# Performance work log

Hardware: AMD Instinct MI355X
Metric: run time of the kernel (lower is better)

The kernel has to match this reference:

```python
import jax, jax.numpy as jnp
import numpy as np

N, IN_DIM, HID, OUT = 8192, 512, 256, 64
NEG_INF = -9e15


def setup_inputs() -> dict:
    key = jax.random.key(0)
    ks = jax.random.split(key, 7)
    X = jax.random.normal(ks[0], (N, IN_DIM), dtype=jnp.float32)
    A = jax.random.randint(ks[1], (N, N), 0, 2, dtype=jnp.int32)
    # fc1 (Linear): kaiming-uniform-ish init, exact dist irrelevant for correctness
    W1 = jax.random.normal(ks[2], (IN_DIM, HID), dtype=jnp.float32) / np.sqrt(IN_DIM)
    b1 = jnp.zeros((HID,), dtype=jnp.float32)
    # attention vector a: xavier_uniform(gain=1.414) on shape (2*HID, 1)
    lim = 1.414 * np.sqrt(6.0 / (2 * HID + 1))
    a = jax.random.uniform(ks[3], (2 * HID, 1), minval=-lim, maxval=lim, dtype=jnp.float32)
    Omega = jax.random.normal(ks[4], (HID, OUT), dtype=jnp.float32) * np.sqrt(2.0 / (HID + OUT))
    beta = jnp.zeros((OUT,), dtype=jnp.float32)
    return {"X": X, "A": A, "W1": W1, "b1": b1, "a": a, "Omega": Omega, "beta": beta}


def reference(X, A, W1, b1, a, Omega, beta):
    H1 = X @ W1 + b1                      # [N, HID]
    # score(i,j) = leakyrelu(a[:HID].H1_i + a[HID:].H1_j) -- computed via broadcast,
    # avoiding the O(N^2 * 2*HID) concat the torch code materializes.
    a1 = a[:HID, 0]                       # [HID]
    a2 = a[HID:, 0]                       # [HID]
    e = jax.nn.leaky_relu((H1 @ a1)[:, None] + (H1 @ a2)[None, :], negative_slope=0.2)  # [N, N]
    e = jnp.where(A > 0, e, NEG_INF)
    attention = jax.nn.softmax(e, axis=1)  # dropout_rate=0.0 -> identity
    H2 = attention @ H1                    # [N, HID]
    return jax.nn.sigmoid(H2 @ Omega + beta)  # [N, OUT]
```

## Files before the change

kernel.cpp:

```cpp
#include <hip/hip_runtime.h>
#include <hip/hip_bf16.h>


typedef float f32x4 __attribute__((ext_vector_type(4)));
typedef short s16x8 __attribute__((ext_vector_type(8)));

#define NN 8192
#define INDIM 512
#define HIDD 256
#define OUTD 64

static __device__ __forceinline__ short f2bf(float x) {
    __hip_bfloat16 h = __float2bfloat16(x);
    return __builtin_bit_cast(short, h);
}

static __device__ __forceinline__ void split_bf(float x, short& hi, short& lo) {
    short h = f2bf(x);
    unsigned int hb = ((unsigned int)(unsigned short)h) << 16;
    float hf = __builtin_bit_cast(float, hb);
    hi = h;
    lo = f2bf(x - hf);
}

__global__ void k_splitW1(const float* __restrict__ W1,
                          short* __restrict__ W1Thi, short* __restrict__ W1Tlo) {
    int t = blockIdx.x * 256 + threadIdx.x;
    int n = t >> 9;
    int k = t & 511;
    float x = W1[k * 256 + n];
    short hi, lo; split_bf(x, hi, lo);
    W1Thi[t] = hi;
    W1Tlo[t] = lo;
}

__global__ void __launch_bounds__(256, 2)
k_h1(const float* __restrict__ X, const short* __restrict__ W1Thi,
     const short* __restrict__ W1Tlo, const float* __restrict__ b1,
     const float* __restrict__ avec, unsigned short* __restrict__ H1TB,
     float* __restrict__ alw, float* __restrict__ bew, float* __restrict__ uvw) {
    __shared__ float s1p[4][16];
    __shared__ float s2p[4][16];
    const int tid = threadIdx.x;
    const int wn = tid >> 6, lane = tid & 63;
    const int q = lane >> 4, m16 = lane & 15;
    const int i0 = blockIdx.x * 16;
    const int irow = i0 + m16;

    f32x4 zero4 = {0.f, 0.f, 0.f, 0.f};
    f32x4 acc[4];
#pragma unroll
    for (int nt = 0; nt < 4; ++nt) acc[nt] = zero4;

    const float* Xrow = X + (size_t)irow * INDIM;
    for (int kk = 0; kk < INDIM; kk += 32) {
        const int k0 = kk + q * 8;
        float4 xa = *(const float4*)(Xrow + k0);
        float4 xb = *(const float4*)(Xrow + k0 + 4);
        float xs[8] = {xa.x, xa.y, xa.z, xa.w, xb.x, xb.y, xb.z, xb.w};
        s16x8 ahi, alo;
#pragma unroll
        for (int j = 0; j < 8; ++j) { short h, l; split_bf(xs[j], h, l); ahi[j] = h; alo[j] = l; }
#pragma unroll
        for (int nt = 0; nt < 4; ++nt) {
            const int n = wn * 64 + nt * 16 + m16;
            s16x8 bhi = *(const s16x8*)(W1Thi + n * INDIM + k0);
            s16x8 blo = *(const s16x8*)(W1Tlo + n * INDIM + k0);
            acc[nt] = __builtin_amdgcn_mfma_f32_16x16x32_bf16(ahi, bhi, acc[nt], 0, 0, 0);
            acc[nt] = __builtin_amdgcn_mfma_f32_16x16x32_bf16(ahi, blo, acc[nt], 0, 0, 0);
            acc[nt] = __builtin_amdgcn_mfma_f32_16x16x32_bf16(alo, bhi, acc[nt], 0, 0, 0);
        }
    }

    float p1[4] = {0.f, 0.f, 0.f, 0.f};
    float p2[4] = {0.f, 0.f, 0.f, 0.f};
    const int rowbase = i0 + q * 4;
    const int chunk = rowbase >> 5, win = rowbase & 31;
#pragma unroll
    for (int nt = 0; nt < 4; ++nt) {
        const int col = wn * 64 + nt * 16 + m16;
        const float b1v = b1[col];
        const float a1v = avec[col];
        const float a2v = avec[HIDD + col];
        float v0 = acc[nt][0] + b1v;
        float v1 = acc[nt][1] + b1v;
        float v2 = acc[nt][2] + b1v;
        float v3 = acc[nt][3] + b1v;
        ushort4 us;
        us.x = (unsigned short)f2bf(v0);
        us.y = (unsigned short)f2bf(v1);
        us.z = (unsigned short)f2bf(v2);
        us.w = (unsigned short)f2bf(v3);
        *(ushort4*)(H1TB + (size_t)chunk * 8192 + col * 32 + win) = us;
        p1[0] += v0 * a1v; p1[1] += v1 * a1v; p1[2] += v2 * a1v; p1[3] += v3 * a1v;
        p2[0] += v0 * a2v; p2[1] += v1 * a2v; p2[2] += v2 * a2v; p2[3] += v3 * a2v;
    }
#pragma unroll
    for (int off = 1; off < 16; off <<= 1) {
#pragma unroll
        for (int r = 0; r < 4; ++r) {
            p1[r] += __shfl_xor(p1[r], off);
            p2[r] += __shfl_xor(p2[r], off);
        }
    }
    if (m16 == 0) {
#pragma unroll
        for (int r = 0; r < 4; ++r) {
            s1p[wn][q * 4 + r] = p1[r];
            s2p[wn][q * 4 + r] = p2[r];
        }
    }
    __syncthreads();
    if (tid < 16) {
        const int i = i0 + tid;
        float s1 = s1p[0][tid] + s1p[1][tid] + s1p[2][tid] + s1p[3][tid];
        float s2 = s2p[0][tid] + s2p[1][tid] + s2p[2][tid] + s2p[3][tid];
        alw[i] = expf(s1);
        bew[i] = expf(0.2f * s1);
        uvw[2 * i]     = expf(s2);
        uvw[2 * i + 1] = expf(0.2f * s2);
    }
}

__global__ void __launch_bounds__(256, 4)
k_attn(const int* __restrict__ A, const unsigned short* __restrict__ H1TB,
       const float* __restrict__ alw, const float* __restrict__ bew,
       const float* __restrict__ uvw,
       float* __restrict__ H2acc, float* __restrict__ Zw) {
    __shared__ unsigned short tile[8192];

    const int tid = threadIdx.x;
    const int wave = tid >> 6, lane = tid & 63;
    const int q = lane >> 4, m16 = lane & 15;
    const int wm = wave & 1, wn = wave >> 1;
    const int mb = blockIdx.x & 255;
    const int ks = blockIdx.x >> 8;
    const int i = mb * 32 + wm * 16 + m16;
    const float al = alw[i], be = bew[i];

    const unsigned short* gp = H1TB + (size_t)ks * 64 * 8192 + tid * 8;
    __attribute__((address_space(3))) unsigned short* tl =
        (__attribute__((address_space(3))) unsigned short*)tile;

    const int* Ap = A + (size_t)i * NN + ks * 2048 + q * 8;
    const float* uvp = uvw + 2 * (ks * 2048 + q * 8);

    f32x4 zero4 = {0.f, 0.f, 0.f, 0.f};
    f32x4 acc[8];
#pragma unroll
    for (int nt = 0; nt < 8; ++nt) acc[nt] = zero4;
    float zacc = 0.f;

    for (int kk = 0; kk < 2048; kk += 32) {
#pragma unroll
        for (int c = 0; c < 4; ++c)
            __builtin_amdgcn_global_load_lds(
                (const __attribute__((address_space(1))) void*)(gp + c * 2048),
                (__attribute__((address_space(3))) void*)(tl + c * 2048 + tid * 8),
                16, 0, 0);
        gp += 8192;

        int4 A0 = *(const int4*)(Ap);
        int4 A1 = *(const int4*)(Ap + 4);
        float4 uv0 = *(const float4*)(uvp);
        float4 uv1 = *(const float4*)(uvp + 4);
        float4 uv2 = *(const float4*)(uvp + 8);
        float4 uv3 = *(const float4*)(uvp + 12);
        Ap += 32; uvp += 64;

        float wv[8];
        wv[0] = (A0.x > 0) ? fmaxf(al * uv0.x, be * uv0.y) : 0.f;
        wv[1] = (A0.y > 0) ? fmaxf(al * uv0.z, be * uv0.w) : 0.f;
        wv[2] = (A0.z > 0) ? fmaxf(al * uv1.x, be * uv1.y) : 0.f;
        wv[3] = (A0.w > 0) ? fmaxf(al * uv1.z, be * uv1.w) : 0.f;
        wv[4] = (A1.x > 0) ? fmaxf(al * uv2.x, be * uv2.y) : 0.f;
        wv[5] = (A1.y > 0) ? fmaxf(al * uv2.z, be * uv2.w) : 0.f;
        wv[6] = (A1.z > 0) ? fmaxf(al * uv3.x, be * uv3.y) : 0.f;
        wv[7] = (A1.w > 0) ? fmaxf(al * uv3.z, be * uv3.w) : 0.f;
        zacc += (wv[0] + wv[1] + wv[2] + wv[3]) + (wv[4] + wv[5] + wv[6] + wv[7]);
        s16x8 af;
#pragma unroll
        for (int j = 0; j < 8; ++j) af[j] = f2bf(wv[j]);

        __syncthreads();
#pragma unroll
        for (int nt = 0; nt < 8; ++nt) {
            s16x8 bf = *(const s16x8*)(tile + (wn * 128 + nt * 16 + m16) * 32 + q * 8);
            acc[nt] = __builtin_amdgcn_mfma_f32_16x16x32_bf16(af, bf, acc[nt], 0, 0, 0);
        }
        __syncthreads();
    }

    zacc += __shfl_xor(zacc, 16);
    zacc += __shfl_xor(zacc, 32);
    if (wn == 0 && q == 0) atomicAdd(&Zw[i], zacc);

    const int rowbase = mb * 32 + wm * 16 + q * 4;
#pragma unroll
    for (int nt = 0; nt < 8; ++nt) {
        const int col = wn * 128 + nt * 16 + m16;
#pragma unroll
        for (int r = 0; r < 4; ++r)
            atomicAdd(&H2acc[(size_t)(rowbase + r) * HIDD + col], acc[nt][r]);
    }
}

__global__ void __launch_bounds__(256)
k_out(const float* __restrict__ H2acc, const float* __restrict__ Zw,
      const float* __restrict__ Omega, const float* __restrict__ beta,
      float* __restrict__ out) {
    __shared__ float om[HIDD * OUTD];
    const int tid = threadIdx.x;
    for (int idx = tid; idx < HIDD * OUTD; idx += 256) om[idx] = Omega[idx];
    __syncthreads();
    const int wave = tid >> 6, o = tid & 63;
    const float bv = beta[o];
    for (int rr = 0; rr < 8; ++rr) {
        const int i = blockIdx.x * 32 + wave * 8 + rr;
        const float4* H2v = (const float4*)(H2acc + (size_t)i * HIDD);
        float acc = 0.f;
#pragma unroll 4
        for (int c4 = 0; c4 < 64; ++c4) {
            float4 h = H2v[c4];
            const int cb = c4 * 4;
            acc = fmaf(h.x, om[(cb + 0) * OUTD + o], acc);
            acc = fmaf(h.y, om[(cb + 1) * OUTD + o], acc);
            acc = fmaf(h.z, om[(cb + 2) * OUTD + o], acc);
            acc = fmaf(h.w, om[(cb + 3) * OUTD + o], acc);
        }
        const float zinv = 1.0f / Zw[i];
        const float logit = acc * zinv + bv;
        out[(size_t)i * OUTD + o] = 1.0f / (1.0f + expf(-logit));
    }
}

extern "C" void kernel_launch(void* const* d_in, const int* in_sizes, int n_in,
                              void* d_out, int out_size, void* d_ws, size_t ws_size,
                              hipStream_t stream) {
    const float* X     = (const float*)d_in[0];
    const int*   A     = (const int*)d_in[1];
    const float* W1    = (const float*)d_in[2];
    const float* b1    = (const float*)d_in[3];
    const float* avec  = (const float*)d_in[4];
    const float* Omega = (const float*)d_in[5];
    const float* beta  = (const float*)d_in[6];
    float* out = (float*)d_out;

    char* ws = (char*)d_ws;
    unsigned short* H1TB = (unsigned short*)(ws + 0);
    short* W1Thi = (short*)(ws + 4194304);
    short* W1Tlo = (short*)(ws + 4456448);
    float* alw   = (float*)(ws + 4718592);
    float* bew   = (float*)(ws + 4751360);
    float* uvw   = (float*)(ws + 4784128);
    float* Zw    = (float*)(ws + 4849664);
    float* H2acc = (float*)(ws + 4882432);

    hipMemsetAsync(Zw, 0, 32768 + 8388608, stream);

    k_splitW1<<<512, 256, 0, stream>>>(W1, W1Thi, W1Tlo);
    k_h1<<<512, 256, 0, stream>>>(X, W1Thi, W1Tlo, b1, avec, H1TB, alw, bew, uvw);
    k_attn<<<1024, 256, 0, stream>>>(A, H1TB, alw, bew, uvw, H2acc, Zw);
    k_out<<<256, 256, 0, stream>>>(H2acc, Zw, Omega, beta, out);
}
```

Baseline: 543.9 us.

## Pre-tile X and W1 into MFMA fragment layout, drop LDS in attention kernel

Adds prep kernels that convert X to bf16 (high part only) and W1 to hi/lo bf16, both stored in MFMA-fragment-contiguous layout, so the H1 GEMM does two MFMAs per step instead of three. The X low part is dropped, which lowers the precision of H1. The attention kernel no longer stages H1 through LDS with barriers. Each wave now handles two row groups and reads B fragments straight from global memory in a blocked layout, with A loads prefetched one step ahead and the K range split into 8 slices. The output kernel is restructured to reuse Omega loads across 8 rows, and the workspace is aliased so XBhi shares space with Zw/H2acc, with the memset moved after k_h1.

Measured after the change: 566.3 us. 1.04x slower.

```diff
diff --git a/kernel.cpp b/kernel.cpp
--- a/kernel.cpp
+++ b/kernel.cpp
@@ -23,20 +23,25 @@
     lo = f2bf(x - hf);
 }
 
-__global__ void k_splitW1(const float* __restrict__ W1,
-                          short* __restrict__ W1Thi, short* __restrict__ W1Tlo) {
+__global__ void k_prepX(const float* __restrict__ X, short* __restrict__ XBhi) {
     int t = blockIdx.x * 256 + threadIdx.x;
-    int n = t >> 9;
-    int k = t & 511;
-    float x = W1[k * 256 + n];
-    short hi, lo; split_bf(x, hi, lo);
-    W1Thi[t] = hi;
-    W1Tlo[t] = lo;
+    int r = t >> 9, k = t & 511;
+    XBhi[(r >> 4) * 8192 + (k >> 3) * 128 + (r & 15) * 8 + (k & 7)] = f2bf(X[t]);
+}
+
+__global__ void k_prepW(const float* __restrict__ W1,
+                        short* __restrict__ WBhi, short* __restrict__ WBlo) {
+    int t = blockIdx.x * 256 + threadIdx.x;
+    int k = t >> 8, n = t & 255;
+    short h, l; split_bf(W1[t], h, l);
+    int idx = (n >> 4) * 8192 + (k >> 3) * 128 + (n & 15) * 8 + (k & 7);
+    WBhi[idx] = h;
+    WBlo[idx] = l;
 }
 
 __global__ void __launch_bounds__(256, 2)
-k_h1(const float* __restrict__ X, const short* __restrict__ W1Thi,
-     const short* __restrict__ W1Tlo, const float* __restrict__ b1,
+k_h1(const short* __restrict__ XBhi, const short* __restrict__ WBhi,
+     const short* __restrict__ WBlo, const float* __restrict__ b1,
      const float* __restrict__ avec, unsigned short* __restrict__ H1TB,
      float* __restrict__ alw, float* __restrict__ bew, float* __restrict__ uvw) {
     __shared__ float s1p[4][16];
@@ -44,38 +49,30 @@
     const int tid = threadIdx.x;
     const int wn = tid >> 6, lane = tid & 63;
     const int q = lane >> 4, m16 = lane & 15;
-    const int i0 = blockIdx.x * 16;
-    const int irow = i0 + m16;
+    const int blk = blockIdx.x;
 
     f32x4 zero4 = {0.f, 0.f, 0.f, 0.f};
     f32x4 acc[4];
 #pragma unroll
     for (int nt = 0; nt < 4; ++nt) acc[nt] = zero4;
 
-    const float* Xrow = X + (size_t)irow * INDIM;
-    for (int kk = 0; kk < INDIM; kk += 32) {
-        const int k0 = kk + q * 8;
-        float4 xa = *(const float4*)(Xrow + k0);
-        float4 xb = *(const float4*)(Xrow + k0 + 4);
-        float xs[8] = {xa.x, xa.y, xa.z, xa.w, xb.x, xb.y, xb.z, xb.w};
-        s16x8 ahi, alo;
-#pragma unroll
-        for (int j = 0; j < 8; ++j) { short h, l; split_bf(xs[j], h, l); ahi[j] = h; alo[j] = l; }
+    const short* xh = XBhi + blk * 8192 + q * 128 + m16 * 8;
+    const short* wh = WBhi + wn * 4 * 8192 + q * 128 + m16 * 8;
+    const short* wl = WBlo + wn * 4 * 8192 + q * 128 + m16 * 8;
+
+    for (int c = 0; c < 16; ++c) {
+        s16x8 ahi = *(const s16x8*)(xh + c * 512);
 #pragma unroll
         for (int nt = 0; nt < 4; ++nt) {
-            const int n = wn * 64 + nt * 16 + m16;
-            s16x8 bhi = *(const s16x8*)(W1Thi + n * INDIM + k0);
-            s16x8 blo = *(const s16x8*)(W1Tlo + n * INDIM + k0);
+            s16x8 bhi = *(const s16x8*)(wh + nt * 8192 + c * 512);
+            s16x8 blo = *(const s16x8*)(wl + nt * 8192 + c * 512);
             acc[nt] = __builtin_amdgcn_mfma_f32_16x16x32_bf16(ahi, bhi, acc[nt], 0, 0, 0);
             acc[nt] = __builtin_amdgcn_mfma_f32_16x16x32_bf16(ahi, blo, acc[nt], 0, 0, 0);
-            acc[nt] = __builtin_amdgcn_mfma_f32_16x16x32_bf16(alo, bhi, acc[nt], 0, 0, 0);
         }
     }
 
     float p1[4] = {0.f, 0.f, 0.f, 0.f};
     float p2[4] = {0.f, 0.f, 0.f, 0.f};
-    const int rowbase = i0 + q * 4;
-    const int chunk = rowbase >> 5, win = rowbase & 31;
 #pragma unroll
     for (int nt = 0; nt < 4; ++nt) {
         const int col = wn * 64 + nt * 16 + m16;
@@ -91,7 +88,9 @@
         us.y = (unsigned short)f2bf(v1);
         us.z = (unsigned short)f2bf(v2);
         us.w = (unsigned short)f2bf(v3);
-        *(ushort4*)(H1TB + (size_t)chunk * 8192 + col * 32 + win) = us;
+        const int idx = ((wn * 4 + nt) * 1024 + blk * 2 + (q >> 1)) * 128
+                        + m16 * 8 + (q & 1) * 4;
+        *(ushort4*)(H1TB + idx) = us;
         p1[0] += v0 * a1v; p1[1] += v1 * a1v; p1[2] += v2 * a1v; p1[3] += v3 * a1v;
         p2[0] += v0 * a2v; p2[1] += v1 * a2v; p2[2] += v2 * a2v; p2[3] += v3 * a2v;
     }
@@ -112,7 +111,7 @@
     }
     __syncthreads();
     if (tid < 16) {
-        const int i = i0 + tid;
+        const int i = blk * 16 + tid;
         float s1 = s1p[0][tid] + s1p[1][tid] + s1p[2][tid] + s1p[3][tid];
         float s2 = s2p[0][tid] + s2p[1][tid] + s2p[2][tid] + s2p[3][tid];
         alw[i] = expf(s1);
@@ -127,81 +126,96 @@
        const float* __restrict__ alw, const float* __restrict__ bew,
        const float* __restrict__ uvw,
        float* __restrict__ H2acc, float* __restrict__ Zw) {
-    __shared__ unsigned short tile[8192];
-
     const int tid = threadIdx.x;
-    const int wave = tid >> 6, lane = tid & 63;
+    const int wn = tid >> 6, lane = tid & 63;
     const int q = lane >> 4, m16 = lane & 15;
-    const int wm = wave & 1, wn = wave >> 1;
-    const int mb = blockIdx.x & 255;
-    const int ks = blockIdx.x >> 8;
-    const int i = mb * 32 + wm * 16 + m16;
-    const float al = alw[i], be = bew[i];
-
-    const unsigned short* gp = H1TB + (size_t)ks * 64 * 8192 + tid * 8;
-    __attribute__((address_space(3))) unsigned short* tl =
-        (__attribute__((address_space(3))) unsigned short*)tile;
-
-    const int* Ap = A + (size_t)i * NN + ks * 2048 + q * 8;
-    const float* uvp = uvw + 2 * (ks * 2048 + q * 8);
+    const int ks = blockIdx.x & 7;
+    const int mb = blockIdx.x >> 3;
+    const int row0 = mb * 32 + m16, row1 = row0 + 16;
+    const float al0 = alw[row0], be0 = bew[row0];
+    const float al1 = alw[row1], be1 = bew[row1];
+    const int j0 = ks * 1024;
+
+    const int* Ap0 = A + (size_t)row0 * NN + j0 + q * 8;
+    const int* Ap1 = A + (size_t)row1 * NN + j0 + q * 8;
+    const float* uvp = uvw + 2 * (j0 + q * 8);
+    const unsigned short* Hp = H1TB + ((size_t)(wn * 4) * 1024 + ks * 128 + q) * 128 + m16 * 8;
 
     f32x4 zero4 = {0.f, 0.f, 0.f, 0.f};
     f32x4 acc[8];
 #pragma unroll
-    for (int nt = 0; nt < 8; ++nt) acc[nt] = zero4;
-    float zacc = 0.f;
-
-    for (int kk = 0; kk < 2048; kk += 32) {
-#pragma unroll
-        for (int c = 0; c < 4; ++c)
-            __builtin_amdgcn_global_load_lds(
-                (const __attribute__((address_space(1))) void*)(gp + c * 2048),
-                (__attribute__((address_space(3))) void*)(tl + c * 2048 + tid * 8),
-                16, 0, 0);
-        gp += 8192;
-
-        int4 A0 = *(const int4*)(Ap);
-        int4 A1 = *(const int4*)(Ap + 4);
+    for (int i = 0; i < 8; ++i) acc[i] = zero4;
+    float z0 = 0.f, z1 = 0.f;
+
+    int4 a00 = *(const int4*)(Ap0);
+    int4 a01 = *(const int4*)(Ap0 + 4);
+    int4 a10 = *(const int4*)(Ap1);
+    int4 a11 = *(const int4*)(Ap1 + 4);
+
+    for (int t = 0; t < 32; ++t) {
+        int4 n00, n01, n10, n11;
+        if (t < 31) {
+            n00 = *(const int4*)(Ap0 + 32);
+            n01 = *(const int4*)(Ap0 + 36);
+            n10 = *(const int4*)(Ap1 + 32);
+            n11 = *(const int4*)(Ap1 + 36);
+        }
         float4 uv0 = *(const float4*)(uvp);
         float4 uv1 = *(const float4*)(uvp + 4);
         float4 uv2 = *(const float4*)(uvp + 8);
         float4 uv3 = *(const float4*)(uvp + 12);
-        Ap += 32; uvp += 64;
-
-        float wv[8];
-        wv[0] = (A0.x > 0) ? fmaxf(al * uv0.x, be * uv0.y) : 0.f;
-        wv[1] = (A0.y > 0) ? fmaxf(al * uv0.z, be * uv0.w) : 0.f;
-        wv[2] = (A0.z > 0) ? fmaxf(al * uv1.x, be * uv1.y) : 0.f;
-        wv[3] = (A0.w > 0) ? fmaxf(al * uv1.z, be * uv1.w) : 0.f;
-        wv[4] = (A1.x > 0) ? fmaxf(al * uv2.x, be * uv2.y) : 0.f;
-        wv[5] = (A1.y > 0) ? fmaxf(al * uv2.z, be * uv2.w) : 0.f;
-        wv[6] = (A1.z > 0) ? fmaxf(al * uv3.x, be * uv3.y) : 0.f;
-        wv[7] = (A1.w > 0) ? fmaxf(al * uv3.z, be * uv3.w) : 0.f;
-        zacc += (wv[0] + wv[1] + wv[2] + wv[3]) + (wv[4] + wv[5] + wv[6] + wv[7]);
-        s16x8 af;
-#pragma unroll
-        for (int j = 0; j < 8; ++j) af[j] = f2bf(wv[j]);
-
-        __syncthreads();
-#pragma unroll
-        for (int nt = 0; nt < 8; ++nt) {
-            s16x8 bf = *(const s16x8*)(tile + (wn * 128 + nt * 16 + m16) * 32 + q * 8);
-            acc[nt] = __builtin_amdgcn_mfma_f32_16x16x32_bf16(af, bf, acc[nt], 0, 0, 0);
-        }
-        __syncthreads();
-    }
-
-    zacc += __shfl_xor(zacc, 16);
-    zacc += __shfl_xor(zacc, 32);
-    if (wn == 0 && q == 0) atomicAdd(&Zw[i], zacc);
-
-    const int rowbase = mb * 32 + wm * 16 + q * 4;
-#pragma unroll
-    for (int nt = 0; nt < 8; ++nt) {
-        const int col = wn * 128 + nt * 16 + m16;
-#pragma unroll
-        for (int r = 0; r < 4; ++r)
-            atomicAdd(&H2acc[(size_t)(rowbase + r) * HIDD + col], acc[nt][r]);
+
+        float w0[8], w1[8];
+        w0[0] = (a00.x > 0) ? fmaxf(al0 * uv0.x, be0 * uv0.y) : 0.f;
+        w0[1] = (a00.y > 0) ? fmaxf(al0 * uv0.z, be0 * uv0.w) : 0.f;
+        w0[2] = (a00.z > 0) ? fmaxf(al0 * uv1.x, be0 * uv1.y) : 0.f;
+        w0[3] = (a00.w > 0) ? fmaxf(al0 * uv1.z, be0 * uv1.w) : 0.f;
+        w0[4] = (a01.x > 0) ? fmaxf(al0 * uv2.x, be0 * uv2.y) : 0.f;
+        w0[5] = (a01.y > 0) ? fmaxf(al0 * uv2.z, be0 * uv2.w) : 0.f;
+        w0[6] = (a01.z > 0) ? fmaxf(al0 * uv3.x, be0 * uv3.y) : 0.f;
+        w0[7] = (a01.w > 0) ? fmaxf(al0 * uv3.z, be0 * uv3.w) : 0.f;
+        w1[0] = (a10.x > 0) ? fmaxf(al1 * uv0.x, be1 * uv0.y) : 0.f;
+        w1[1] = (a10.y > 0) ? fmaxf(al1 * uv0.z, be1 * uv0.w) : 0.f;
+        w1[2] = (a10.z > 0) ? fmaxf(al1 * uv1.x, be1 * uv1.y) : 0.f;
+        w1[3] = (a10.w > 0) ? fmaxf(al1 * uv1.z, be1 * uv1.w) : 0.f;
+        w1[4] = (a11.x > 0) ? fmaxf(al1 * uv2.x, be1 * uv2.y) : 0.f;
+        w1[5] = (a11.y > 0) ? fmaxf(al1 * uv2.z, be1 * uv2.w) : 0.f;
+        w1[6] = (a11.z > 0) ? fmaxf(al1 * uv3.x, be1 * uv3.y) : 0.f;
+        w1[7] = (a11.w > 0) ? fmaxf(al1 * uv3.z, be1 * uv3.w) : 0.f;
+        z0 += (w0[0] + w0[1] + w0[2] + w0[3]) + (w0[4] + w0[5] + w0[6] + w0[7]);
+        z1 += (w1[0] + w1[1] + w1[2] + w1[3]) + (w1[4] + w1[5] + w1[6] + w1[7]);
+
+        s16x8 af0, af1;
+#pragma unroll
+        for (int j = 0; j < 8; ++j) { af0[j] = f2bf(w0[j]); af1[j] = f2bf(w1[j]); }
+
+#pragma unroll
+        for (int nt = 0; nt < 4; ++nt) {
+            s16x8 bf = *(const s16x8*)(Hp + (size_t)nt * 131072 + t * 512);
+            acc[nt * 2 + 0] = __builtin_amdgcn_mfma_f32_16x16x32_bf16(af0, bf, acc[nt * 2 + 0], 0, 0, 0);
+            acc[nt * 2 + 1] = __builtin_amdgcn_mfma_f32_16x16x32_bf16(af1, bf, acc[nt * 2 + 1], 0, 0, 0);
+        }
+        if (t < 31) { a00 = n00; a01 = n01; a10 = n10; a11 = n11; }
+        Ap0 += 32; Ap1 += 32; uvp += 64;
+    }
+
+    z0 += __shfl_xor(z0, 16); z0 += __shfl_xor(z0, 32);
+    z1 += __shfl_xor(z1, 16); z1 += __shfl_xor(z1, 32);
+    if (wn == 0 && q == 0) {
+        atomicAdd(&Zw[row0], z0);
+        atomicAdd(&Zw[row1], z1);
+    }
+
+#pragma unroll
+    for (int nt = 0; nt < 4; ++nt) {
+        const int col = wn * 64 + nt * 16 + m16;
+#pragma unroll
+        for (int rg = 0; rg < 2; ++rg) {
+            const int rowb = mb * 32 + rg * 16 + q * 4;
+#pragma unroll
+            for (int r = 0; r < 4; ++r)
+                atomicAdd(&H2acc[(size_t)(rowb + r) * HIDD + col], acc[nt * 2 + rg][r]);
+        }
     }
 }
 
@@ -214,23 +228,24 @@
     for (int idx = tid; idx < HIDD * OUTD; idx += 256) om[idx] = Omega[idx];
     __syncthreads();
     const int wave = tid >> 6, o = tid & 63;
+    const int i0 = blockIdx.x * 32 + wave * 8;
+    float acc[8] = {0.f, 0.f, 0.f, 0.f, 0.f, 0.f, 0.f, 0.f};
+    for (int c = 0; c < HIDD; c += 4) {
+        const float o0 = om[(c + 0) * OUTD + o];
+        const float o1 = om[(c + 1) * OUTD + o];
+        const float o2 = om[(c + 2) * OUTD + o];
+        const float o3 = om[(c + 3) * OUTD + o];
+#pragma unroll
+        for (int r = 0; r < 8; ++r) {
+            float4 h = *(const float4*)(H2acc + (size_t)(i0 + r) * HIDD + c);
+            acc[r] = fmaf(h.x, o0, fmaf(h.y, o1, fmaf(h.z, o2, fmaf(h.w, o3, acc[r]))));
+        }
+    }
     const float bv = beta[o];
-    for (int rr = 0; rr < 8; ++rr) {
-        const int i = blockIdx.x * 32 + wave * 8 + rr;
-        const float4* H2v = (const float4*)(H2acc + (size_t)i * HIDD);
-        float acc = 0.f;
-#pragma unroll 4
-        for (int c4 = 0; c4 < 64; ++c4) {
-            float4 h = H2v[c4];
-            const int cb = c4 * 4;
-            acc = fmaf(h.x, om[(cb + 0) * OUTD + o], acc);
-            acc = fmaf(h.y, om[(cb + 1) * OUTD + o], acc);
-            acc = fmaf(h.z, om[(cb + 2) * OUTD + o], acc);
-            acc = fmaf(h.w, om[(cb + 3) * OUTD + o], acc);
-        }
-        const float zinv = 1.0f / Zw[i];
-        const float logit = acc * zinv + bv;
-        out[(size_t)i * OUTD + o] = 1.0f / (1.0f + expf(-logit));
+#pragma unroll
+    for (int r = 0; r < 8; ++r) {
+        const float logit = acc[r] / Zw[i0 + r] + bv;
+        out[(size_t)(i0 + r) * OUTD + o] = 1.0f / (1.0f + expf(-logit));
     }
 }
 
@@ -248,18 +263,19 @@
 
     char* ws = (char*)d_ws;
     unsigned short* H1TB = (unsigned short*)(ws + 0);
-    short* W1Thi = (short*)(ws + 4194304);
-    short* W1Tlo = (short*)(ws + 4456448);
-    float* alw   = (float*)(ws + 4718592);
-    float* bew   = (float*)(ws + 4751360);
-    float* uvw   = (float*)(ws + 4784128);
-    float* Zw    = (float*)(ws + 4849664);
-    float* H2acc = (float*)(ws + 4882432);
-
+    short* XBhi  = (short*)(ws + 4194304);
+    float* Zw    = (float*)(ws + 4194304);
+    float* H2acc = (float*)(ws + 4227072);
+    short* WBhi  = (short*)(ws + 12615680);
+    short* WBlo  = (short*)(ws + 12877824);
+    float* alw   = (float*)(ws + 13139968);
+    float* bew   = (float*)(ws + 13172736);
+    float* uvw   = (float*)(ws + 13205504);
+
+    k_prepX<<<16384, 256, 0, stream>>>(X, XBhi);
+    k_prepW<<<512, 256, 0, stream>>>(W1, WBhi, WBlo);
+    k_h1<<<512, 256, 0, stream>>>(XBhi, WBhi, WBlo, b1, avec, H1TB, alw, bew, uvw);
     hipMemsetAsync(Zw, 0, 32768 + 8388608, stream);
-
-    k_splitW1<<<512, 256, 0, stream>>>(W1, W1Thi, W1Tlo);
-    k_h1<<<512, 256, 0, stream>>>(X, W1Thi, W1Tlo, b1, avec, H1TB, alw, bew, uvw);
-    k_attn<<<1024, 256, 0, stream>>>(A, H1TB, alw, bew, uvw, H2acc, Zw);
+    k_attn<<<2048, 256, 0, stream>>>(A, H1TB, alw, bew, uvw, H2acc, Zw);
     k_out<<<256, 256, 0, stream>>>(H2acc, Zw, Omega, beta, out);
 }
```
